# Performance work log

Hardware: AMD Instinct MI355X
Metric: run time of the kernel (lower is better)

The kernel has to match this reference:

```python
import jax, jax.numpy as jnp
import numpy as np

B, T, IN, H, HORIZON = 1024, 256, 128, 128, 24


def setup_inputs() -> dict:
    key = jax.random.key(0)
    ks = jax.random.split(key, 10)
    def init(k, shape, fan_in):
        return jax.random.normal(k, shape, jnp.float32) / np.sqrt(fan_in)
    return {
        "x": jax.random.normal(ks[0], (B, T, IN), jnp.float32),
        # haiku hk.GRU params: w_i [in, 3H], w_h [H, 3H], b [3H]
        "w_i": init(ks[1], (IN, 3 * H), IN),
        "w_h": init(ks[2], (H, 3 * H), H),
        "b": jnp.zeros((3 * H,), jnp.float32),
        # MLP: single Linear H -> 4H (no final activation)
        "mlp_w": init(ks[3], (H, 4 * H), H),
        "mlp_b": jnp.zeros((4 * H,), jnp.float32),
        # fc: Linear(T*4H -> H) after flatten
        "fc_w": init(ks[4], (T * 4 * H, H), T * 4 * H),
        "fc_b": jnp.zeros((H,), jnp.float32),
        # fc_out: Linear(H -> horizon)
        "out_w": init(ks[5], (H, HORIZON), H),
        "out_b": jnp.zeros((HORIZON,), jnp.float32),
    }


def reference(x, w_i, w_h, b, mlp_w, mlp_b, fc_w, fc_b, out_w, out_b):
    h_dim = w_h.shape[0]
    w_h_zr, w_h_a = w_h[:, : 2 * h_dim], w_h[:, 2 * h_dim :]
    b_zr, b_a = b[: 2 * h_dim], b[2 * h_dim :]

    def step(h, xt):  # h: [B,H], xt: [B,IN]  (haiku hk.GRU math)
        gx = xt @ w_i  # [B,3H]
        zr = jax.nn.sigmoid(gx[:, : 2 * h_dim] + h @ w_h_zr + b_zr)
        z, r = zr[:, :h_dim], zr[:, h_dim:]
        a = jnp.tanh(gx[:, 2 * h_dim :] + (r * h) @ w_h_a + b_a)
        h_new = (1.0 - z) * h + z * a
        return h_new, h_new

    h0 = jnp.zeros((x.shape[0], h_dim), x.dtype)
    _, ys = jax.lax.scan(step, h0, jnp.swapaxes(x, 0, 1))  # ys: [T,B,H]
    ys = jnp.swapaxes(ys, 0, 1)  # [B,T,H]
    y = ys @ mlp_w + mlp_b  # [B,T,4H]
    y = y.reshape(x.shape[0], -1)  # [B, T*4H]
    y = y @ fc_w + fc_b  # [B,H]
    return y @ out_w + out_b  # [B,horizon]
```

## Files before the change

kernel.cpp:

```cpp
#include <hip/hip_runtime.h>
#include <hip/hip_bf16.h>

typedef __bf16 bf16x8 __attribute__((ext_vector_type(8)));
typedef float f32x4 __attribute__((ext_vector_type(4)));

#define MFMA16(A, B, C) __builtin_amdgcn_mfma_f32_16x16x32_bf16((A), (B), (C), 0, 0, 0)

#define BARRIER_LDS() do { \
    asm volatile("s_waitcnt lgkmcnt(0)" ::: "memory"); \
    __builtin_amdgcn_s_barrier(); \
  } while (0)

namespace {
constexpr int kT = 256, kIN = 128, kHZ = 24;
}

__device__ __forceinline__ float fsig(float v) {
  float e = __builtin_amdgcn_exp2f(-1.44269504088896340736f * v);
  return __builtin_amdgcn_rcpf(1.0f + e);
}
__device__ __forceinline__ float ftanh(float v) {
  float e = __builtin_amdgcn_exp2f(2.88539008177792681472f * v);
  return 1.0f - 2.0f * __builtin_amdgcn_rcpf(e + 1.0f);
}

template<int XF>
__global__ __launch_bounds__(256, 1) void gru_main(
    const float* __restrict__ x, const __bf16* __restrict__ xfrag,
    const float* __restrict__ w_i, const float* __restrict__ w_h,
    const float* __restrict__ bias, const __bf16* __restrict__ Nfrag,
    const float* __restrict__ cvec, float* __restrict__ out)
{
  const int tid = threadIdx.x;
  const int w = tid >> 6;
  const int l = tid & 63;
  const int lrow = l & 15;
  const int lg = l >> 4;
  const int b0 = blockIdx.x * 16;

  __shared__ __align__(16) __bf16 h_bf[16 * 128];
  __shared__ __align__(16) __bf16 rh_bf[16 * 128];
  __shared__ __align__(16) float red[4][2][64][4];

  for (int i = tid; i < 16 * 128; i += 256) { h_bf[i] = (__bf16)0.0f; rh_bf[i] = (__bf16)0.0f; }

  bf16x8 Wzr[8][4];
  bf16x8 Wa[8][2];
#pragma unroll
  for (int kc = 0; kc < 8; ++kc) {
#pragma unroll
    for (int nt = 0; nt < 4; ++nt) {
      const int col = (nt < 2) ? (w * 32 + nt * 16 + lrow)
                               : (128 + w * 32 + (nt - 2) * 16 + lrow);
      bf16x8 f;
#pragma unroll
      for (int e = 0; e < 8; ++e) {
        const int k = kc * 32 + lg * 8 + e;
        const float v = (k < 128) ? w_i[k * 384 + col] : w_h[(k - 128) * 384 + col];
        f[e] = (__bf16)v;
      }
      Wzr[kc][nt] = f;
    }
  }
#pragma unroll
  for (int kc = 0; kc < 8; ++kc) {
#pragma unroll
    for (int nt = 0; nt < 2; ++nt) {
      const int col = 256 + w * 32 + nt * 16 + lrow;
      bf16x8 f;
#pragma unroll
      for (int e = 0; e < 8; ++e) {
        const int k = kc * 32 + lg * 8 + e;
        const float v = (k < 128) ? w_i[k * 384 + col] : w_h[(k - 128) * 384 + col];
        f[e] = (__bf16)v;
      }
      Wa[kc][nt] = f;
    }
  }

  float bz[2], br[2], ba[2];
#pragma unroll
  for (int nt = 0; nt < 2; ++nt) {
    bz[nt] = bias[w * 32 + nt * 16 + lrow];
    br[nt] = bias[128 + w * 32 + nt * 16 + lrow];
    ba[nt] = bias[256 + w * 32 + nt * 16 + lrow];
  }

  float hreg[2][4] = {{0.f,0.f,0.f,0.f},{0.f,0.f,0.f,0.f}};
  float zreg[2][4];

  const __bf16* nl = Nfrag + (size_t)w * 1024 + (size_t)l * 8;
  const __bf16* xl = xfrag + (size_t)blockIdx.x * kT * 2048 + (size_t)l * 8;
  const float* xbase = x + ((size_t)(b0 + lrow)) * kT * kIN + lg * 8;

  f32x4 oacc[2] = {{0.f,0.f,0.f,0.f},{0.f,0.f,0.f,0.f}};
  f32x4 xacc1[4], xacc2[2];
  bf16x8 xfA[4], xfB[4], hf[4], rf[4], nCur[2], nB[2];

  auto load_x = [&](bf16x8 dst[4], int t) {
    if (XF) {
      const __bf16* xp = xl + (size_t)t * 2048;
#pragma unroll
      for (int kc = 0; kc < 4; ++kc) dst[kc] = *(const bf16x8*)(xp + kc * 512);
    } else {
#pragma unroll
      for (int kc = 0; kc < 4; ++kc) {
        const float4* p = (const float4*)(xbase + (size_t)t * kIN + kc * 32);
        const float4 a = p[0], b = p[1];
        bf16x8 f;
        f[0]=(__bf16)a.x; f[1]=(__bf16)a.y; f[2]=(__bf16)a.z; f[3]=(__bf16)a.w;
        f[4]=(__bf16)b.x; f[5]=(__bf16)b.y; f[6]=(__bf16)b.z; f[7]=(__bf16)b.w;
        dst[kc] = f;
      }
    }
  };
  auto compute_xacc = [&](const bf16x8 xv[4]) {
#pragma unroll
    for (int nt = 0; nt < 2; ++nt) {
      f32x4 a = {bz[nt], bz[nt], bz[nt], bz[nt]}; xacc1[nt] = a;
      f32x4 b = {br[nt], br[nt], br[nt], br[nt]}; xacc1[2 + nt] = b;
      f32x4 c = {ba[nt], ba[nt], ba[nt], ba[nt]}; xacc2[nt] = c;
    }
#pragma unroll
    for (int kc = 0; kc < 4; ++kc) {
#pragma unroll
      for (int nt = 0; nt < 4; ++nt) xacc1[nt] = MFMA16(xv[kc], Wzr[kc][nt], xacc1[nt]);
#pragma unroll
      for (int nt = 0; nt < 2; ++nt) xacc2[nt] = MFMA16(xv[kc], Wa[kc][nt], xacc2[nt]);
    }
  };

  {
    bf16x8 xv0[4];
    load_x(xv0, 0);
    compute_xacc(xv0);
  }
  load_x(xfA, 1);
  load_x(xfB, 2);
  nCur[0] = *(const bf16x8*)(nl);
  nCur[1] = *(const bf16x8*)(nl + 512);
  nB[0] = nCur[0]; nB[1] = nCur[1];

  __syncthreads();

#pragma unroll 1
  for (int t = 0; t < kT; ++t) {
#pragma unroll
    for (int kc = 0; kc < 4; ++kc) {
      const int idx = (lrow * 128 + kc * 32 + lg * 8) ^ ((lrow & 7) << 3);
      hf[kc] = *(const bf16x8*)(h_bf + idx);
    }
    f32x4 acc1[4];
#pragma unroll
    for (int nt = 0; nt < 4; ++nt) acc1[nt] = xacc1[nt];
#pragma unroll
    for (int kc = 0; kc < 4; ++kc) {
#pragma unroll
      for (int nt = 0; nt < 4; ++nt) acc1[nt] = MFMA16(hf[kc], Wzr[kc + 4][nt], acc1[nt]);
    }
    oacc[0] = MFMA16(hf[w], nCur[0], oacc[0]);
    oacc[1] = MFMA16(hf[w], nCur[1], oacc[1]);
    nCur[0] = nB[0]; nCur[1] = nB[1];
    {
      const int tn = (t < kT - 1) ? (t + 1) : (kT - 1);
      const __bf16* np = nl + (size_t)tn * 4096;
      nB[0] = *(const bf16x8*)(np);
      nB[1] = *(const bf16x8*)(np + 512);
    }
#pragma unroll
    for (int nt = 0; nt < 2; ++nt) {
#pragma unroll
      for (int j = 0; j < 4; ++j) {
        const float rr = fsig(acc1[2 + nt][j]);
        const float rh = rr * hreg[nt][j];
        const int row = lg * 4 + j;
        const int col = w * 32 + nt * 16 + lrow;
        rh_bf[(row * 128 + col) ^ ((row & 7) << 3)] = (__bf16)rh;
      }
    }
#pragma unroll
    for (int nt = 0; nt < 2; ++nt) {
#pragma unroll
      for (int j = 0; j < 4; ++j) zreg[nt][j] = fsig(acc1[nt][j]);
    }
    BARRIER_LDS();
#pragma unroll
    for (int kc = 0; kc < 4; ++kc) {
      const int idx = (lrow * 128 + kc * 32 + lg * 8) ^ ((lrow & 7) << 3);
      rf[kc] = *(const bf16x8*)(rh_bf + idx);
    }
    f32x4 acc2[2];
#pragma unroll
    for (int nt = 0; nt < 2; ++nt) acc2[nt] = xacc2[nt];
#pragma unroll
    for (int kc = 0; kc < 4; ++kc) {
#pragma unroll
      for (int nt = 0; nt < 2; ++nt) acc2[nt] = MFMA16(rf[kc], Wa[kc + 4][nt], acc2[nt]);
    }
    compute_xacc(xfA);
#pragma unroll
    for (int nt = 0; nt < 2; ++nt) {
#pragma unroll
      for (int j = 0; j < 4; ++j) {
        const float a = ftanh(acc2[nt][j]);
        const float hn = fmaf(zreg[nt][j], a - hreg[nt][j], hreg[nt][j]);
        hreg[nt][j] = hn;
        const int row = lg * 4 + j;
        const int col = w * 32 + nt * 16 + lrow;
        h_bf[(row * 128 + col) ^ ((row & 7) << 3)] = (__bf16)hn;
      }
    }
#pragma unroll
    for (int kc = 0; kc < 4; ++kc) xfA[kc] = xfB[kc];
    {
      const int tn = (t + 3 < kT) ? (t + 3) : (kT - 1);
      load_x(xfB, tn);
    }
    BARRIER_LDS();
  }

  {
    const int idx = (lrow * 128 + w * 32 + lg * 8) ^ ((lrow & 7) << 3);
    bf16x8 hlast = *(const bf16x8*)(h_bf + idx);
    oacc[0] = MFMA16(hlast, nCur[0], oacc[0]);
    oacc[1] = MFMA16(hlast, nCur[1], oacc[1]);
  }
  *(f32x4*)(&red[w][0][l][0]) = oacc[0];
  *(f32x4*)(&red[w][1][l][0]) = oacc[1];
  __syncthreads();
  if (w < 2) {
    const int nt = w;
#pragma unroll
    for (int j = 0; j < 4; ++j) {
      const int row = lg * 4 + j;
      const int col = nt * 16 + lrow;
      if (col < kHZ) {
        const float v = red[0][nt][l][j] + red[1][nt][l][j] +
                        red[2][nt][l][j] + red[3][nt][l][j] + cvec[col];
        out[(size_t)(b0 + row) * kHZ + col] = v;
      }
    }
  }
}

__global__ __launch_bounds__(256) void xprep(
    const float* __restrict__ x, __bf16* __restrict__ xfrag)
{
  const int bg = blockIdx.x, t = blockIdx.y;
  const int tid = threadIdx.x;
  const int kc = tid >> 6, l = tid & 63;
  const int row = l & 15, lgx = l >> 4;
  const float* src = x + (((size_t)(bg * 16 + row)) * kT + t) * kIN + kc * 32 + lgx * 8;
  const float4 a = ((const float4*)src)[0];
  const float4 b = ((const float4*)src)[1];
  bf16x8 f;
  f[0]=(__bf16)a.x; f[1]=(__bf16)a.y; f[2]=(__bf16)a.z; f[3]=(__bf16)a.w;
  f[4]=(__bf16)b.x; f[5]=(__bf16)b.y; f[6]=(__bf16)b.z; f[7]=(__bf16)b.w;
  *(bf16x8*)(xfrag + ((size_t)bg * kT + t) * 2048 + (size_t)tid * 8) = f;
}

__global__ __launch_bounds__(256) void nprep(
    const float* __restrict__ mlp_w, const float* __restrict__ fc_w,
    const float* __restrict__ out_w, __bf16* __restrict__ Nfrag)
{
  const int t = blockIdx.x;
  const int tid = threadIdx.x;
  __shared__ __align__(16) float Q[512 * 24];
  __shared__ __align__(16) float obuf[4096];

  float* ow = obuf;
  for (int i = tid; i < 128 * 24; i += 256) ow[i] = out_w[i];
  __syncthreads();

  for (int i = tid; i < 512; i += 256) {
    const float* rowp = fc_w + ((size_t)t * 512 + i) * 128;
    float q[24];
#pragma unroll
    for (int j = 0; j < 24; ++j) q[j] = 0.0f;
    auto acc_m = [&](float rv, int m) {
      const float4* owp = (const float4*)(ow + m * 24);
      const float4 o0 = owp[0], o1 = owp[1], o2 = owp[2];
      const float4 o3 = owp[3], o4 = owp[4], o5 = owp[5];
      q[0]  = fmaf(rv, o0.x, q[0]);  q[1]  = fmaf(rv, o0.y, q[1]);
      q[2]  = fmaf(rv, o0.z, q[2]);  q[3]  = fmaf(rv, o0.w, q[3]);
      q[4]  = fmaf(rv, o1.x, q[4]);  q[5]  = fmaf(rv, o1.y, q[5]);
      q[6]  = fmaf(rv, o1.z, q[6]);  q[7]  = fmaf(rv, o1.w, q[7]);
      q[8]  = fmaf(rv, o2.x, q[8]);  q[9]  = fmaf(rv, o2.y, q[9]);
      q[10] = fmaf(rv, o2.z, q[10]); q[11] = fmaf(rv, o2.w, q[11]);
      q[12] = fmaf(rv, o3.x, q[12]); q[13] = fmaf(rv, o3.y, q[13]);
      q[14] = fmaf(rv, o3.z, q[14]); q[15] = fmaf(rv, o3.w, q[15]);
      q[16] = fmaf(rv, o4.x, q[16]); q[17] = fmaf(rv, o4.y, q[17]);
      q[18] = fmaf(rv, o4.z, q[18]); q[19] = fmaf(rv, o4.w, q[19]);
      q[20] = fmaf(rv, o5.x, q[20]); q[21] = fmaf(rv, o5.y, q[21]);
      q[22] = fmaf(rv, o5.z, q[22]); q[23] = fmaf(rv, o5.w, q[23]);
    };
#pragma unroll 4
    for (int m4 = 0; m4 < 32; ++m4) {
      const float4 rv = *(const float4*)(rowp + m4 * 4);
      acc_m(rv.x, m4 * 4 + 0);
      acc_m(rv.y, m4 * 4 + 1);
      acc_m(rv.z, m4 * 4 + 2);
      acc_m(rv.w, m4 * 4 + 3);
    }
#pragma unroll
    for (int j = 0; j < 24; ++j) Q[i * 24 + j] = q[j];
  }
  __syncthreads();

  {
    const int i = tid & 127;
    const int jh = tid >> 7;
    const float* mrow = mlp_w + (size_t)i * 512;
    float q[12];
#pragma unroll
    for (int j = 0; j < 12; ++j) q[j] = 0.0f;
    auto acc_k = [&](float mv, int k) {
      const float* qrow = Q + (size_t)k * 24 + jh * 12;
      const float4 q0 = *(const float4*)(qrow);
      const float4 q1 = *(const float4*)(qrow + 4);
      const float4 q2 = *(const float4*)(qrow + 8);
      q[0]  = fmaf(mv, q0.x, q[0]);  q[1]  = fmaf(mv, q0.y, q[1]);
      q[2]  = fmaf(mv, q0.z, q[2]);  q[3]  = fmaf(mv, q0.w, q[3]);
      q[4]  = fmaf(mv, q1.x, q[4]);  q[5]  = fmaf(mv, q1.y, q[5]);
      q[6]  = fmaf(mv, q1.z, q[6]);  q[7]  = fmaf(mv, q1.w, q[7]);
      q[8]  = fmaf(mv, q2.x, q[8]);  q[9]  = fmaf(mv, q2.y, q[9]);
      q[10] = fmaf(mv, q2.z, q[10]); q[11] = fmaf(mv, q2.w, q[11]);
    };
#pragma unroll 2
    for (int k4 = 0; k4 < 128; ++k4) {
      const float4 mv = *(const float4*)(mrow + k4 * 4);
      acc_k(mv.x, k4 * 4 + 0);
      acc_k(mv.y, k4 * 4 + 1);
      acc_k(mv.z, k4 * 4 + 2);
      acc_k(mv.w, k4 * 4 + 3);
    }
    float* Nb = obuf;
#pragma unroll
    for (int j = 0; j < 12; ++j) Nb[i * 32 + jh * 12 + j] = q[j];
  }
  for (int idx = tid; idx < 128 * 8; idx += 256) obuf[(idx >> 3) * 32 + 24 + (idx & 7)] = 0.0f;
  __syncthreads();

  {
    const float* Nb = obuf;
#pragma unroll
    for (int u = 0; u < 16; ++u) {
      const int f = tid * 16 + u;
      const int e = f & 7;
      const int lane = (f >> 3) & 63;
      const int nt = (f >> 9) & 1;
      const int kc = f >> 10;
      const int k = kc * 32 + (lane >> 4) * 8 + e;
      const int colj = nt * 16 + (lane & 15);
      Nfrag[(size_t)t * 4096 + f] = (__bf16)Nb[k * 32 + colj];
    }
  }
}

__global__ __launch_bounds__(256) void bias_partial(
    const float* __restrict__ mlp_b, const float* __restrict__ fc_w,
    float* __restrict__ partial)
{
  const int r0 = blockIdx.x;
  const int tid = threadIdx.x;
  const int m = tid & 127;
  const int g = tid >> 7;
  __shared__ int anynz;
  if (tid == 0) anynz = 0;
  __syncthreads();
  {
    int nz = 0;
    for (int i = tid; i < 512; i += 256) nz |= (mlp_b[i] != 0.0f) ? 1 : 0;
    if (nz) atomicOr(&anynz, 1);
  }
  __syncthreads();
  float acc = 0.0f;
  if (anynz) {
    for (int i = g; i < 512; i += 2)
      acc = fmaf(mlp_b[i], fc_w[((size_t)r0 * 512 + i) * 128 + m], acc);
  }
  __shared__ float sred[2][128];
  sred[g][m] = acc;
  __syncthreads();
  if (g == 0) partial[r0 * 128 + m] = sred[0][m] + sred[1][m];
}

__global__ __launch_bounds__(128) void bias_final(
    const float* __restrict__ fc_b, const float* __restrict__ out_b,
    const float* __restrict__ out_w, const float* __restrict__ partial,
    float* __restrict__ cvec)
{
  const int m = threadIdx.x;
  float s = fc_b[m];
  for (int r0 = 0; r0 < 256; ++r0) s += partial[r0 * 128 + m];
  __shared__ float sm[128];
  sm[m] = s;
  __syncthreads();
  if (m < kHZ) {
    float c = out_b[m];
    for (int k = 0; k < 128; ++k) c = fmaf(sm[k], out_w[k * kHZ + m], c);
    cvec[m] = c;
  }
}

extern "C" void kernel_launch(void* const* d_in, const int* in_sizes, int n_in,
                              void* d_out, int out_size, void* d_ws, size_t ws_size,
                              hipStream_t stream) {
  (void)in_sizes; (void)n_in; (void)out_size;
  const float* x     = (const float*)d_in[0];
  const float* w_i   = (const float*)d_in[1];
  const float* w_h   = (const float*)d_in[2];
  const float* bias  = (const float*)d_in[3];
  const float* mlp_w = (const float*)d_in[4];
  const float* mlp_b = (const float*)d_in[5];
  const float* fc_w  = (const float*)d_in[6];
  const float* fc_b  = (const float*)d_in[7];
  const float* out_w = (const float*)d_in[8];
  const float* out_b = (const float*)d_in[9];
  float* out = (float*)d_out;

  const size_t nfrag_b   = (size_t)256 * 4096 * 2;
  const size_t partial_b = (size_t)256 * 128 * 4;
  const size_t cvec_b    = 4096;
  const size_t xfrag_b   = (size_t)64 * 256 * 2048 * 2;
  __bf16* Nfrag  = (__bf16*)d_ws;
  float* partial = (float*)((char*)d_ws + nfrag_b);
  float* cvec    = (float*)((char*)d_ws + nfrag_b + partial_b);
  __bf16* xfrag  = (__bf16*)((char*)d_ws + nfrag_b + partial_b + cvec_b);
  const bool use_xf = ws_size >= nfrag_b + partial_b + cvec_b + xfrag_b;

  nprep<<<256, 256, 0, stream>>>(mlp_w, fc_w, out_w, Nfrag);
  bias_partial<<<256, 256, 0, stream>>>(mlp_b, fc_w, partial);
  bias_final<<<1, 128, 0, stream>>>(fc_b, out_b, out_w, partial, cvec);
  if (use_xf) {
    xprep<<<dim3(64, 256), 256, 0, stream>>>(x, xfrag);
    gru_main<1><<<64, 256, 0, stream>>>(x, xfrag, w_i, w_h, bias, Nfrag, cvec, out);
  } else {
    gru_main<0><<<64, 256, 0, stream>>>(x, xfrag, w_i, w_h, bias, Nfrag, cvec, out);
  }
}
```

Before: 649.2 us.

## Precompute input-gate GEMM in parallel kernel and pack two batch groups per block

Adds a parallel gx_gemm kernel that computes x@w_i+bias for all timesteps up front and stores it as bf16 in MFMA-fragment layout. A new recurrent kernel gru2 then only runs the hidden-state matmuls per step, reading the precomputed gate inputs with a one-step register prefetch. It also packs two 16-row batch groups into one 512-thread block. This takes the input projection off the serial critical path at the cost of a large bf16 workspace buffer and the extra bf16 rounding of the gate pre-activations.

```diff
diff --git a/kernel.cpp b/kernel.cpp
--- a/kernel.cpp
+++ b/kernel.cpp
@@ -2,6 +2,7 @@
 #include <hip/hip_bf16.h>
 
 typedef __bf16 bf16x8 __attribute__((ext_vector_type(8)));
+typedef __bf16 bf16x4 __attribute__((ext_vector_type(4)));
 typedef float f32x4 __attribute__((ext_vector_type(4)));
 
 #define MFMA16(A, B, C) __builtin_amdgcn_mfma_f32_16x16x32_bf16((A), (B), (C), 0, 0, 0)
@@ -22,6 +23,240 @@
 __device__ __forceinline__ float ftanh(float v) {
   float e = __builtin_amdgcn_exp2f(2.88539008177792681472f * v);
   return 1.0f - 2.0f * __builtin_amdgcn_rcpf(e + 1.0f);
+}
+__device__ __forceinline__ f32x4 bf4_to_f32(uint2 u) {
+  f32x4 r;
+  r[0] = __uint_as_float(u.x << 16);
+  r[1] = __uint_as_float(u.x & 0xffff0000u);
+  r[2] = __uint_as_float(u.y << 16);
+  r[3] = __uint_as_float(u.y & 0xffff0000u);
+  return r;
+}
+
+__global__ __launch_bounds__(512, 2) void gru2(
+    const __bf16* __restrict__ gxf, const float* __restrict__ w_h,
+    const __bf16* __restrict__ Nfrag, const float* __restrict__ cvec,
+    float* __restrict__ out)
+{
+  const int tid = threadIdx.x;
+  const int w8 = tid >> 6;
+  const int l = tid & 63;
+  const int grp = w8 >> 2;
+  const int w = w8 & 3;
+  const int lrow = l & 15;
+  const int lg = l >> 4;
+  const int gidx = blockIdx.x * 2 + grp;
+  const int b0 = gidx * 16;
+
+  __shared__ __align__(16) __bf16 h_bf[2][16 * 128];
+  __shared__ __align__(16) __bf16 rh_bf[2][16 * 128];
+  __shared__ __align__(16) float red[2][4][2][64][4];
+
+  for (int i = tid; i < 2 * 16 * 128; i += 512) {
+    ((__bf16*)h_bf)[i] = (__bf16)0.0f;
+    ((__bf16*)rh_bf)[i] = (__bf16)0.0f;
+  }
+
+  bf16x8 Wzr[4][4];
+  bf16x8 Wa[4][2];
+#pragma unroll
+  for (int kc = 0; kc < 4; ++kc) {
+#pragma unroll
+    for (int nt = 0; nt < 4; ++nt) {
+      const int col = (nt < 2) ? (w * 32 + nt * 16 + lrow)
+                               : (128 + w * 32 + (nt - 2) * 16 + lrow);
+      bf16x8 f;
+#pragma unroll
+      for (int e = 0; e < 8; ++e) f[e] = (__bf16)w_h[(kc * 32 + lg * 8 + e) * 384 + col];
+      Wzr[kc][nt] = f;
+    }
+#pragma unroll
+    for (int nt = 0; nt < 2; ++nt) {
+      const int col = 256 + w * 32 + nt * 16 + lrow;
+      bf16x8 f;
+#pragma unroll
+      for (int e = 0; e < 8; ++e) f[e] = (__bf16)w_h[(kc * 32 + lg * 8 + e) * 384 + col];
+      Wa[kc][nt] = f;
+    }
+  }
+
+  float hreg[2][4] = {{0.f,0.f,0.f,0.f},{0.f,0.f,0.f,0.f}};
+  float zreg[2][4];
+  f32x4 oacc[2] = {{0.f,0.f,0.f,0.f},{0.f,0.f,0.f,0.f}};
+
+  const __bf16* nl = Nfrag + (size_t)w * 1024 + (size_t)l * 8;
+  const __bf16* gxl = gxf + ((size_t)gidx * 256 * 4 + (size_t)w) * 1536 + (size_t)l * 4;
+
+  bf16x8 hf[4], rf[4], nCur[2], nB[2];
+  uint2 gxA[6], gxB[6];
+
+#pragma unroll
+  for (int i = 0; i < 6; ++i) gxA[i] = *(const uint2*)(gxl + i * 256);
+  nCur[0] = *(const bf16x8*)(nl);
+  nCur[1] = *(const bf16x8*)(nl + 512);
+  nB[0] = nCur[0]; nB[1] = nCur[1];
+
+  __syncthreads();
+
+#pragma unroll 1
+  for (int t = 0; t < kT; ++t) {
+    const int tn = (t < kT - 1) ? (t + 1) : (kT - 1);
+    {
+      const __bf16* gp = gxl + (size_t)tn * 6144;
+#pragma unroll
+      for (int i = 0; i < 6; ++i) gxB[i] = *(const uint2*)(gp + i * 256);
+    }
+#pragma unroll
+    for (int kc = 0; kc < 4; ++kc) {
+      const int idx = (lrow * 128 + kc * 32 + lg * 8) ^ ((lrow & 7) << 3);
+      hf[kc] = *(const bf16x8*)(&h_bf[grp][0] + idx);
+    }
+    f32x4 acc1[4];
+#pragma unroll
+    for (int nt = 0; nt < 4; ++nt) acc1[nt] = bf4_to_f32(gxA[nt]);
+#pragma unroll
+    for (int kc = 0; kc < 4; ++kc) {
+#pragma unroll
+      for (int nt = 0; nt < 4; ++nt) acc1[nt] = MFMA16(hf[kc], Wzr[kc][nt], acc1[nt]);
+    }
+    oacc[0] = MFMA16(hf[w], nCur[0], oacc[0]);
+    oacc[1] = MFMA16(hf[w], nCur[1], oacc[1]);
+    nCur[0] = nB[0]; nCur[1] = nB[1];
+    {
+      const __bf16* np = nl + (size_t)tn * 4096;
+      nB[0] = *(const bf16x8*)(np);
+      nB[1] = *(const bf16x8*)(np + 512);
+    }
+#pragma unroll
+    for (int nt = 0; nt < 2; ++nt) {
+#pragma unroll
+      for (int j = 0; j < 4; ++j) {
+        const float rr = fsig(acc1[2 + nt][j]);
+        const float rh = rr * hreg[nt][j];
+        const int row = lg * 4 + j;
+        const int col = w * 32 + nt * 16 + lrow;
+        rh_bf[grp][(row * 128 + col) ^ ((row & 7) << 3)] = (__bf16)rh;
+      }
+    }
+#pragma unroll
+    for (int nt = 0; nt < 2; ++nt) {
+#pragma unroll
+      for (int j = 0; j < 4; ++j) zreg[nt][j] = fsig(acc1[nt][j]);
+    }
+    BARRIER_LDS();
+#pragma unroll
+    for (int kc = 0; kc < 4; ++kc) {
+      const int idx = (lrow * 128 + kc * 32 + lg * 8) ^ ((lrow & 7) << 3);
+      rf[kc] = *(const bf16x8*)(&rh_bf[grp][0] + idx);
+    }
+    f32x4 acc2[2];
+#pragma unroll
+    for (int nt = 0; nt < 2; ++nt) acc2[nt] = bf4_to_f32(gxA[4 + nt]);
+#pragma unroll
+    for (int kc = 0; kc < 4; ++kc) {
+#pragma unroll
+      for (int nt = 0; nt < 2; ++nt) acc2[nt] = MFMA16(rf[kc], Wa[kc][nt], acc2[nt]);
+    }
+#pragma unroll
+    for (int nt = 0; nt < 2; ++nt) {
+#pragma unroll
+      for (int j = 0; j < 4; ++j) {
+        const float a = ftanh(acc2[nt][j]);
+        const float hn = fmaf(zreg[nt][j], a - hreg[nt][j], hreg[nt][j]);
+        hreg[nt][j] = hn;
+        const int row = lg * 4 + j;
+        const int col = w * 32 + nt * 16 + lrow;
+        h_bf[grp][(row * 128 + col) ^ ((row & 7) << 3)] = (__bf16)hn;
+      }
+    }
+#pragma unroll
+    for (int i = 0; i < 6; ++i) gxA[i] = gxB[i];
+    BARRIER_LDS();
+  }
+
+  {
+    const int idx = (lrow * 128 + w * 32 + lg * 8) ^ ((lrow & 7) << 3);
+    bf16x8 hlast = *(const bf16x8*)(&h_bf[grp][0] + idx);
+    oacc[0] = MFMA16(hlast, nCur[0], oacc[0]);
+    oacc[1] = MFMA16(hlast, nCur[1], oacc[1]);
+  }
+  *(f32x4*)(&red[grp][w][0][l][0]) = oacc[0];
+  *(f32x4*)(&red[grp][w][1][l][0]) = oacc[1];
+  __syncthreads();
+  if (w < 2) {
+    const int nt = w;
+#pragma unroll
+    for (int j = 0; j < 4; ++j) {
+      const int row = lg * 4 + j;
+      const int col = nt * 16 + lrow;
+      if (col < kHZ) {
+        const float v = red[grp][0][nt][l][j] + red[grp][1][nt][l][j] +
+                        red[grp][2][nt][l][j] + red[grp][3][nt][l][j] + cvec[col];
+        out[(size_t)(b0 + row) * kHZ + col] = v;
+      }
+    }
+  }
+}
+
+__global__ __launch_bounds__(256) void gx_gemm(
+    const float* __restrict__ x, const float* __restrict__ w_i,
+    const float* __restrict__ bias, __bf16* __restrict__ gxf)
+{
+  const int g = blockIdx.x;
+  const int tq = blockIdx.y;
+  const int tid = threadIdx.x;
+  const int w = tid >> 6, l = tid & 63;
+  const int lrow = l & 15, lg = l >> 4;
+
+  bf16x8 Wf[4][6];
+  float bs[6];
+#pragma unroll
+  for (int nt = 0; nt < 6; ++nt) {
+    const int col = w * 96 + nt * 16 + lrow;
+    bs[nt] = bias[col];
+#pragma unroll
+    for (int kc = 0; kc < 4; ++kc) {
+      bf16x8 f;
+#pragma unroll
+      for (int e = 0; e < 8; ++e) f[e] = (__bf16)w_i[(kc * 32 + lg * 8 + e) * 384 + col];
+      Wf[kc][nt] = f;
+    }
+  }
+
+#pragma unroll 1
+  for (int it = 0; it < 4; ++it) {
+    const int t = tq * 4 + it;
+    const float* xp = x + (((size_t)(g * 16 + lrow)) * kT + t) * kIN + lg * 8;
+    bf16x8 af[4];
+#pragma unroll
+    for (int kc = 0; kc < 4; ++kc) {
+      const float4 a = *(const float4*)(xp + kc * 32);
+      const float4 b = *(const float4*)(xp + kc * 32 + 4);
+      bf16x8 f;
+      f[0]=(__bf16)a.x; f[1]=(__bf16)a.y; f[2]=(__bf16)a.z; f[3]=(__bf16)a.w;
+      f[4]=(__bf16)b.x; f[5]=(__bf16)b.y; f[6]=(__bf16)b.z; f[7]=(__bf16)b.w;
+      af[kc] = f;
+    }
+    f32x4 acc[6];
+#pragma unroll
+    for (int nt = 0; nt < 6; ++nt) { f32x4 a = {bs[nt], bs[nt], bs[nt], bs[nt]}; acc[nt] = a; }
+#pragma unroll
+    for (int kc = 0; kc < 4; ++kc) {
+#pragma unroll
+      for (int nt = 0; nt < 6; ++nt) acc[nt] = MFMA16(af[kc], Wf[kc][nt], acc[nt]);
+    }
+#pragma unroll
+    for (int nt = 0; nt < 6; ++nt) {
+      const int ct = w * 6 + nt;
+      const int gate = ct >> 3;
+      const int wp = (ct & 7) >> 1;
+      const int slot = gate * 2 + (ct & 1);
+      bf16x4 o;
+      o[0]=(__bf16)acc[nt][0]; o[1]=(__bf16)acc[nt][1];
+      o[2]=(__bf16)acc[nt][2]; o[3]=(__bf16)acc[nt][3];
+      *(bf16x4*)(gxf + (((size_t)g * 256 + t) * 4 + wp) * 1536 + slot * 256 + l * 4) = o;
+    }
+  }
 }
 
 template<int XF>
@@ -422,20 +657,27 @@
   const size_t nfrag_b   = (size_t)256 * 4096 * 2;
   const size_t partial_b = (size_t)256 * 128 * 4;
   const size_t cvec_b    = 4096;
+  const size_t base_b    = nfrag_b + partial_b + cvec_b;
+  const size_t gxf_b     = (size_t)64 * 256 * 4 * 1536 * 2;
   const size_t xfrag_b   = (size_t)64 * 256 * 2048 * 2;
   __bf16* Nfrag  = (__bf16*)d_ws;
   float* partial = (float*)((char*)d_ws + nfrag_b);
   float* cvec    = (float*)((char*)d_ws + nfrag_b + partial_b);
-  __bf16* xfrag  = (__bf16*)((char*)d_ws + nfrag_b + partial_b + cvec_b);
-  const bool use_xf = ws_size >= nfrag_b + partial_b + cvec_b + xfrag_b;
+  char*  bufp    = (char*)d_ws + base_b;
 
   nprep<<<256, 256, 0, stream>>>(mlp_w, fc_w, out_w, Nfrag);
   bias_partial<<<256, 256, 0, stream>>>(mlp_b, fc_w, partial);
   bias_final<<<1, 128, 0, stream>>>(fc_b, out_b, out_w, partial, cvec);
-  if (use_xf) {
+
+  if (ws_size >= base_b + gxf_b) {
+    __bf16* gxf = (__bf16*)bufp;
+    gx_gemm<<<dim3(64, 64), 256, 0, stream>>>(x, w_i, bias, gxf);
+    gru2<<<32, 512, 0, stream>>>(gxf, w_h, Nfrag, cvec, out);
+  } else if (ws_size >= base_b + xfrag_b) {
+    __bf16* xfrag = (__bf16*)bufp;
     xprep<<<dim3(64, 256), 256, 0, stream>>>(x, xfrag);
     gru_main<1><<<64, 256, 0, stream>>>(x, xfrag, w_i, w_h, bias, Nfrag, cvec, out);
   } else {
-    gru_main<0><<<64, 256, 0, stream>>>(x, xfrag, w_i, w_h, bias, Nfrag, cvec, out);
-  }
-}
+    gru_main<0><<<64, 256, 0, stream>>>(x, (const __bf16*)bufp, w_i, w_h, bias, Nfrag, cvec, out);
+  }
+}
```

After: 1.027 ms. 1.58x slower.
